# Optimization experiments

Hardware: AMD Instinct MI355X
Metric: run time of the kernel (lower is better)

Reference implementation:

```python
import jax, jax.numpy as jnp
import numpy as np

CODEBOOK_SIZE = 512
LATENT_DIM = 12
BATCH = 512
TOKENS = 256


def setup_inputs() -> dict:
    key = jax.random.key(0)
    k1, k2 = jax.random.split(key)
    x = jax.random.normal(k1, (BATCH, TOKENS, LATENT_DIM), dtype=jnp.float32)
    # nn.Embedding init: uniform(-1/K, 1/K)
    lim = 1.0 / CODEBOOK_SIZE
    codebook = jax.random.uniform(k2, (CODEBOOK_SIZE, LATENT_DIM), dtype=jnp.float32,
                                  minval=-lim, maxval=lim)
    return {"x": x, "codebook": codebook}


def reference(x, codebook):
    # same as for torch.cdist (sqrt is monotonic).
    x2 = jnp.sum(x * x, axis=-1, keepdims=True)            # [B, N, 1]
    w2 = jnp.sum(codebook * codebook, axis=-1)             # [K]
    xw = jnp.einsum('bnd,kd->bnk', x, codebook)            # [B, N, K]
    dist2 = x2 - 2.0 * xw + w2                             # [B, N, K]
    indices = jnp.argmin(dist2, axis=-1)                   # [B, N] int
    quantized = codebook[indices]                          # [B, N, D]

    codebook_loss = jnp.mean((quantized - jax.lax.stop_gradient(x)) ** 2)
    commitment_loss = 0.25 * jnp.mean((jax.lax.stop_gradient(quantized) - x) ** 2)
    quantize_loss = codebook_loss + commitment_loss

    # straight-through estimator
    quantized_st = x + jax.lax.stop_gradient(quantized - x)
    return quantized_st, indices, quantize_loss
```

## Files before the change

kernel.cpp:

```cpp
#include <hip/hip_runtime.h>
#include <math.h>

namespace {
constexpr int KCB   = 512;
constexpr int DIM   = 12;
constexpr int NTOK  = 512 * 256;
constexpr int QSIZE = NTOK * DIM;
constexpr int NSPLIT = 4;
constexpr int KCHUNK = KCB / NSPLIT;
constexpr int TOKS_PER_BLOCK = 64;

__global__ __launch_bounds__(256) void pack_cb(const float* __restrict__ cb,
                                               float* __restrict__ pk,
                                               float* __restrict__ out) {
    int k = blockIdx.x * blockDim.x + threadIdx.x;
    if (k == 0) out[QSIZE + NTOK] = 0.f;
    if (k >= KCB) return;
    float w[DIM];
#pragma unroll
    for (int d = 0; d < DIM; ++d) w[d] = cb[k * DIM + d];
    float w2 = 0.f;
#pragma unroll
    for (int d = 0; d < DIM; ++d) w2 += w[d] * w[d];
#pragma unroll
    for (int d = 0; d < DIM; ++d) pk[k * 16 + d] = w[d];
    pk[k * 16 + 12] = w2;
    pk[k * 16 + 13] = 0.f;
    pk[k * 16 + 14] = 0.f;
    pk[k * 16 + 15] = 0.f;
}

__global__ __launch_bounds__(256, 8) void vq_main(const float* __restrict__ x,
                                                  const float* __restrict__ cb,
                                                  const float4* __restrict__ pk,
                                                  float* __restrict__ out) {
    const int tid  = threadIdx.x;
    const int lane = tid & 63;
    const int s = __builtin_amdgcn_readfirstlane(tid >> 6);
    const int t = blockIdx.x * TOKS_PER_BLOCK + lane;

    const float4* xp = (const float4*)(x + (size_t)t * DIM);
    float4 xa = xp[0], xb = xp[1], xc = xp[2];
    float xs[DIM] = {xa.x, xa.y, xa.z, xa.w,
                     xb.x, xb.y, xb.z, xb.w,
                     xc.x, xc.y, xc.z, xc.w};

    float x2 = 0.f;
#pragma unroll
    for (int d = 0; d < DIM; ++d) x2 = fmaf(xs[d], xs[d], x2);

    float best = INFINITY;
    int bi = 0;
    const int k0 = s * KCHUNK;
#pragma unroll 4
    for (int kk = 0; kk < KCHUNK; ++kk) {
        const int k = k0 + kk;
        float4 c0 = pk[k * 4 + 0];
        float4 c1 = pk[k * 4 + 1];
        float4 c2 = pk[k * 4 + 2];
        float4 c3 = pk[k * 4 + 3];
        float xw = 0.f;
        xw = fmaf(xs[0],  c0.x, xw);
        xw = fmaf(xs[1],  c0.y, xw);
        xw = fmaf(xs[2],  c0.z, xw);
        xw = fmaf(xs[3],  c0.w, xw);
        xw = fmaf(xs[4],  c1.x, xw);
        xw = fmaf(xs[5],  c1.y, xw);
        xw = fmaf(xs[6],  c1.z, xw);
        xw = fmaf(xs[7],  c1.w, xw);
        xw = fmaf(xs[8],  c2.x, xw);
        xw = fmaf(xs[9],  c2.y, xw);
        xw = fmaf(xs[10], c2.z, xw);
        xw = fmaf(xs[11], c2.w, xw);
        float dsc = fmaf(-2.f, xw, x2) + c3.x;
        bool cnd = dsc < best;
        best = cnd ? dsc : best;
        bi   = cnd ? k : bi;
    }

    unsigned su = __float_as_uint(best);
    su = (su & 0x80000000u) ? ~su : (su | 0x80000000u);
    unsigned long long key = ((unsigned long long)su << 32) | (unsigned)bi;

    __shared__ unsigned long long red[NSPLIT][TOKS_PER_BLOCK];
    red[s][lane] = key;
    __syncthreads();

    if (s == 0) {
        unsigned long long m0 = red[0][lane], m1 = red[1][lane];
        unsigned long long m2 = red[2][lane], m3 = red[3][lane];
        unsigned long long a = m0 < m1 ? m0 : m1;
        unsigned long long b = m2 < m3 ? m2 : m3;
        unsigned long long m = a < b ? a : b;
        const int bid = (int)(m & 0xffffffffULL);
        unsigned eu = (unsigned)(m >> 32);
        unsigned orig = (eu & 0x80000000u) ? (eu ^ 0x80000000u) : ~eu;
        const float bsc = __uint_as_float(orig);

        const float4* wrow = (const float4*)(cb + (size_t)bid * DIM);
        float4 q0 = wrow[0], q1 = wrow[1], q2 = wrow[2];
        float qs[DIM] = {q0.x, q0.y, q0.z, q0.w,
                         q1.x, q1.y, q1.z, q1.w,
                         q2.x, q2.y, q2.z, q2.w};
        float4* qo = (float4*)(out + (size_t)t * DIM);
        float4 r0, r1, r2;
        r0.x = xs[0] + (qs[0] - xs[0]);    r0.y = xs[1] + (qs[1] - xs[1]);
        r0.z = xs[2] + (qs[2] - xs[2]);    r0.w = xs[3] + (qs[3] - xs[3]);
        r1.x = xs[4] + (qs[4] - xs[4]);    r1.y = xs[5] + (qs[5] - xs[5]);
        r1.z = xs[6] + (qs[6] - xs[6]);    r1.w = xs[7] + (qs[7] - xs[7]);
        r2.x = xs[8] + (qs[8] - xs[8]);    r2.y = xs[9] + (qs[9] - xs[9]);
        r2.z = xs[10] + (qs[10] - xs[10]); r2.w = xs[11] + (qs[11] - xs[11]);
        qo[0] = r0; qo[1] = r1; qo[2] = r2;

        out[QSIZE + t] = (float)bid;

        float ls = bsc * (1.25f / (float)QSIZE);
#pragma unroll
        for (int off = 32; off > 0; off >>= 1) ls += __shfl_down(ls, off);
        if (lane == 0) atomicAdd(out + QSIZE + NTOK, ls);
    }
}
}

extern "C" void kernel_launch(void* const* d_in, const int* in_sizes, int n_in,
                              void* d_out, int out_size, void* d_ws, size_t ws_size,
                              hipStream_t stream) {
    const float* x  = (const float*)d_in[0];
    const float* cb = (const float*)d_in[1];
    float* out = (float*)d_out;
    float* pk  = (float*)d_ws;

    pack_cb<<<2, 256, 0, stream>>>(cb, pk, out);
    vq_main<<<NTOK / TOKS_PER_BLOCK, 256, 0, stream>>>(x, cb, (const float4*)pk, out);
}
```

Before: 109.5 us.

## Process two tokens per thread and split codebook across eight waves

Each thread now scores two tokens against the same codebook entries, so every codebook load feeds twice the FMAs. Blocks grow to 512 threads with eight waves, each scanning a 64-entry slice, and the shared-memory reduction now merges eight partial minima per token. An inline-asm zero is added to the codebook pointer, which appears meant to force per-lane vector loads instead of scalar loads. The cost is doubled register state per thread and fewer resident blocks per CU.

```diff
diff --git a/kernel.cpp b/kernel.cpp
--- a/kernel.cpp
+++ b/kernel.cpp
@@ -6,9 +6,11 @@
 constexpr int DIM   = 12;
 constexpr int NTOK  = 512 * 256;
 constexpr int QSIZE = NTOK * DIM;
-constexpr int NSPLIT = 4;
+constexpr int NSPLIT = 8;
 constexpr int KCHUNK = KCB / NSPLIT;
-constexpr int TOKS_PER_BLOCK = 64;
+constexpr int TPT    = 2;
+constexpr int TOKS_PER_BLOCK = 64 * TPT;
+constexpr int NBLK   = NTOK / TOKS_PER_BLOCK;
 
 __global__ __launch_bounds__(256) void pack_cb(const float* __restrict__ cb,
                                                float* __restrict__ pk,
@@ -30,87 +32,116 @@
     pk[k * 16 + 15] = 0.f;
 }
 
-__global__ __launch_bounds__(256, 8) void vq_main(const float* __restrict__ x,
+__device__ inline void code_score(const float (&xv)[DIM], float x2,
+                                  const float4& c0, const float4& c1,
+                                  const float4& c2, const float4& c3,
+                                  float& dsc) {
+    float xw = 0.f;
+    xw = fmaf(xv[0],  c0.x, xw);
+    xw = fmaf(xv[1],  c0.y, xw);
+    xw = fmaf(xv[2],  c0.z, xw);
+    xw = fmaf(xv[3],  c0.w, xw);
+    xw = fmaf(xv[4],  c1.x, xw);
+    xw = fmaf(xv[5],  c1.y, xw);
+    xw = fmaf(xv[6],  c1.z, xw);
+    xw = fmaf(xv[7],  c1.w, xw);
+    xw = fmaf(xv[8],  c2.x, xw);
+    xw = fmaf(xv[9],  c2.y, xw);
+    xw = fmaf(xv[10], c2.z, xw);
+    xw = fmaf(xv[11], c2.w, xw);
+    dsc = fmaf(-2.f, xw, x2) + c3.x;
+}
+
+__global__ __launch_bounds__(512, 4) void vq_main(const float* __restrict__ x,
                                                   const float* __restrict__ cb,
                                                   const float4* __restrict__ pk,
                                                   float* __restrict__ out) {
     const int tid  = threadIdx.x;
     const int lane = tid & 63;
     const int s = __builtin_amdgcn_readfirstlane(tid >> 6);
-    const int t = blockIdx.x * TOKS_PER_BLOCK + lane;
+    const int tA = blockIdx.x * TOKS_PER_BLOCK + lane;
+    const int tB = tA + 64;
 
-    const float4* xp = (const float4*)(x + (size_t)t * DIM);
-    float4 xa = xp[0], xb = xp[1], xc = xp[2];
-    float xs[DIM] = {xa.x, xa.y, xa.z, xa.w,
-                     xb.x, xb.y, xb.z, xb.w,
-                     xc.x, xc.y, xc.z, xc.w};
+    int dz;
+    asm volatile("v_mov_b32 %0, 0" : "=v"(dz));
+    const float4* pkd = pk + (size_t)(unsigned)dz;
 
-    float x2 = 0.f;
+    const float4* xpA = (const float4*)(x + (size_t)tA * DIM);
+    const float4* xpB = (const float4*)(x + (size_t)tB * DIM);
+    float4 a0 = xpA[0], a1 = xpA[1], a2 = xpA[2];
+    float4 b0 = xpB[0], b1 = xpB[1], b2 = xpB[2];
+    float xsA[DIM] = {a0.x, a0.y, a0.z, a0.w, a1.x, a1.y, a1.z, a1.w,
+                      a2.x, a2.y, a2.z, a2.w};
+    float xsB[DIM] = {b0.x, b0.y, b0.z, b0.w, b1.x, b1.y, b1.z, b1.w,
+                      b2.x, b2.y, b2.z, b2.w};
+
+    float x2A = 0.f, x2B = 0.f;
 #pragma unroll
-    for (int d = 0; d < DIM; ++d) x2 = fmaf(xs[d], xs[d], x2);
+    for (int d = 0; d < DIM; ++d) x2A = fmaf(xsA[d], xsA[d], x2A);
+#pragma unroll
+    for (int d = 0; d < DIM; ++d) x2B = fmaf(xsB[d], xsB[d], x2B);
 
-    float best = INFINITY;
-    int bi = 0;
+    float bestA = INFINITY, bestB = INFINITY;
+    int biA = 0, biB = 0;
     const int k0 = s * KCHUNK;
-#pragma unroll 4
+    const float4* cp = pkd + (size_t)k0 * 4;
+#pragma unroll 2
     for (int kk = 0; kk < KCHUNK; ++kk) {
+        float4 c0 = cp[0], c1 = cp[1], c2 = cp[2], c3 = cp[3];
+        cp += 4;
         const int k = k0 + kk;
-        float4 c0 = pk[k * 4 + 0];
-        float4 c1 = pk[k * 4 + 1];
-        float4 c2 = pk[k * 4 + 2];
-        float4 c3 = pk[k * 4 + 3];
-        float xw = 0.f;
-        xw = fmaf(xs[0],  c0.x, xw);
-        xw = fmaf(xs[1],  c0.y, xw);
-        xw = fmaf(xs[2],  c0.z, xw);
-        xw = fmaf(xs[3],  c0.w, xw);
-        xw = fmaf(xs[4],  c1.x, xw);
-        xw = fmaf(xs[5],  c1.y, xw);
-        xw = fmaf(xs[6],  c1.z, xw);
-        xw = fmaf(xs[7],  c1.w, xw);
-        xw = fmaf(xs[8],  c2.x, xw);
-        xw = fmaf(xs[9],  c2.y, xw);
-        xw = fmaf(xs[10], c2.z, xw);
-        xw = fmaf(xs[11], c2.w, xw);
-        float dsc = fmaf(-2.f, xw, x2) + c3.x;
-        bool cnd = dsc < best;
-        best = cnd ? dsc : best;
-        bi   = cnd ? k : bi;
+        float dA, dB;
+        code_score(xsA, x2A, c0, c1, c2, c3, dA);
+        code_score(xsB, x2B, c0, c1, c2, c3, dB);
+        bool cA = dA < bestA;
+        bestA = cA ? dA : bestA;
+        biA   = cA ? k : biA;
+        bool cB = dB < bestB;
+        bestB = cB ? dB : bestB;
+        biB   = cB ? k : biB;
     }
 
-    unsigned su = __float_as_uint(best);
-    su = (su & 0x80000000u) ? ~su : (su | 0x80000000u);
-    unsigned long long key = ((unsigned long long)su << 32) | (unsigned)bi;
-
+    auto mkkey = [](float v, int k) {
+        unsigned su = __float_as_uint(v);
+        su = (su & 0x80000000u) ? ~su : (su | 0x80000000u);
+        return ((unsigned long long)su << 32) | (unsigned)k;
+    };
     __shared__ unsigned long long red[NSPLIT][TOKS_PER_BLOCK];
-    red[s][lane] = key;
+    red[s][lane]      = mkkey(bestA, biA);
+    red[s][64 + lane] = mkkey(bestB, biB);
     __syncthreads();
 
-    if (s == 0) {
-        unsigned long long m0 = red[0][lane], m1 = red[1][lane];
-        unsigned long long m2 = red[2][lane], m3 = red[3][lane];
-        unsigned long long a = m0 < m1 ? m0 : m1;
-        unsigned long long b = m2 < m3 ? m2 : m3;
-        unsigned long long m = a < b ? a : b;
+    if (s < TPT) {
+        const int tok = s * 64 + lane;
+        unsigned long long m = red[0][tok];
+#pragma unroll
+        for (int r = 1; r < NSPLIT; ++r) {
+            unsigned long long v = red[r][tok];
+            m = v < m ? v : m;
+        }
         const int bid = (int)(m & 0xffffffffULL);
         unsigned eu = (unsigned)(m >> 32);
         unsigned orig = (eu & 0x80000000u) ? (eu ^ 0x80000000u) : ~eu;
         const float bsc = __uint_as_float(orig);
+        const int t = blockIdx.x * TOKS_PER_BLOCK + tok;
 
         const float4* wrow = (const float4*)(cb + (size_t)bid * DIM);
         float4 q0 = wrow[0], q1 = wrow[1], q2 = wrow[2];
-        float qs[DIM] = {q0.x, q0.y, q0.z, q0.w,
-                         q1.x, q1.y, q1.z, q1.w,
+        float qs[DIM] = {q0.x, q0.y, q0.z, q0.w, q1.x, q1.y, q1.z, q1.w,
                          q2.x, q2.y, q2.z, q2.w};
-        float4* qo = (float4*)(out + (size_t)t * DIM);
-        float4 r0, r1, r2;
-        r0.x = xs[0] + (qs[0] - xs[0]);    r0.y = xs[1] + (qs[1] - xs[1]);
-        r0.z = xs[2] + (qs[2] - xs[2]);    r0.w = xs[3] + (qs[3] - xs[3]);
-        r1.x = xs[4] + (qs[4] - xs[4]);    r1.y = xs[5] + (qs[5] - xs[5]);
-        r1.z = xs[6] + (qs[6] - xs[6]);    r1.w = xs[7] + (qs[7] - xs[7]);
-        r2.x = xs[8] + (qs[8] - xs[8]);    r2.y = xs[9] + (qs[9] - xs[9]);
-        r2.z = xs[10] + (qs[10] - xs[10]); r2.w = xs[11] + (qs[11] - xs[11]);
-        qo[0] = r0; qo[1] = r1; qo[2] = r2;
+
+        auto emit = [&](const float (&xv)[DIM]) {
+            float4* qo = (float4*)(out + (size_t)t * DIM);
+            float4 r0, r1, r2;
+            r0.x = xv[0] + (qs[0] - xv[0]);    r0.y = xv[1] + (qs[1] - xv[1]);
+            r0.z = xv[2] + (qs[2] - xv[2]);    r0.w = xv[3] + (qs[3] - xv[3]);
+            r1.x = xv[4] + (qs[4] - xv[4]);    r1.y = xv[5] + (qs[5] - xv[5]);
+            r1.z = xv[6] + (qs[6] - xv[6]);    r1.w = xv[7] + (qs[7] - xv[7]);
+            r2.x = xv[8] + (qs[8] - xv[8]);    r2.y = xv[9] + (qs[9] - xv[9]);
+            r2.z = xv[10] + (qs[10] - xv[10]); r2.w = xv[11] + (qs[11] - xv[11]);
+            qo[0] = r0; qo[1] = r1; qo[2] = r2;
+        };
+        if (s == 0) emit(xsA); else emit(xsB);
 
         out[QSIZE + t] = (float)bid;
 
@@ -131,5 +162,5 @@
     float* pk  = (float*)d_ws;
 
     pack_cb<<<2, 256, 0, stream>>>(cb, pk, out);
-    vq_main<<<NTOK / TOKS_PER_BLOCK, 256, 0, stream>>>(x, cb, (const float4*)pk, out);
+    vq_main<<<NBLK, 512, 0, stream>>>(x, cb, (const float4*)pk, out);
 }
```

Measured after the change: 137.9 us. 1.26x slower.
